# Kernel optimization log

Measured on AMD Instinct MI355X. Metric: run time of the kernel, lower is better.

## Reference

```python
import jax, jax.numpy as jnp
import numpy as np

HEADS, DH = 8, 64  # SelfAttention defaults: heads=8, dim_head=64


def _layernorm(x, g, b, eps=1e-5):
    mu = x.mean(-1, keepdims=True)
    var = ((x - mu) ** 2).mean(-1, keepdims=True)
    return (x - mu) / jnp.sqrt(var + eps) * g + b


def setup_inputs() -> dict:
    key = jax.random.key(0)
    ks = jax.random.split(key, 13)
    B, H, W, D, P = 1, 256, 256, 64, 128
    inner = HEADS * DH
    s = 0.05  # weight scale to keep logits in a sane range
    return {
        "x": jax.random.normal(ks[0], (B, H, W, D), jnp.float32),
        "pair_bias": jax.random.normal(ks[1], (B, W, W, P), jnp.float32),
        "Wq_w": jax.random.normal(ks[2], (D, inner), jnp.float32) * s,
        "Wkv_w": jax.random.normal(ks[3], (D, 2 * inner), jnp.float32) * s,
        "Wout_w": jax.random.normal(ks[4], (inner, D), jnp.float32) * s,
        "bout_w": jnp.zeros((D,), jnp.float32),
        "Wq_h": jax.random.normal(ks[5], (D, inner), jnp.float32) * s,
        "Wkv_h": jax.random.normal(ks[6], (D, 2 * inner), jnp.float32) * s,
        "Wout_h": jax.random.normal(ks[7], (inner, D), jnp.float32) * s,
        "bout_h": jnp.zeros((D,), jnp.float32),
        "pair_ln_g": jnp.ones((P,), jnp.float32),
        "pair_ln_b": jnp.zeros((P,), jnp.float32),
        "W_pair": jax.random.normal(ks[8], (P, HEADS), jnp.float32) * s,
    }


def _qkv(x2d, Wq, Wkv):
    # x2d: (N, L, D) -> q, k, v each (N, heads, L, dh)
    N, L, _ = x2d.shape
    q = (x2d @ Wq).reshape(N, L, HEADS, DH).transpose(0, 2, 1, 3)
    kv = (x2d @ Wkv).reshape(N, L, 2, HEADS, DH)
    k = kv[:, :, 0].transpose(0, 2, 1, 3)
    v = kv[:, :, 1].transpose(0, 2, 1, 3)
    return q, k, v


def reference(x, pair_bias, Wq_w, Wkv_w, Wout_w, bout_w,
              Wq_h, Wkv_h, Wout_h, bout_h, pair_ln_g, pair_ln_b, W_pair):
    B, H, W, D = x.shape  # B=1, H=n_seqs, W=length, D=dim
    scale = DH ** -0.5

    # ---- width attention: attend over seq dim H, batched per column (b*w) ----
    xw = jnp.transpose(x, (0, 2, 1, 3)).reshape(B * W, H, D)
    q, k, v = _qkv(xw, Wq_w, Wkv_w)
    dots = jnp.einsum('bhid,bhjd->bhij', q, k) * scale  # (B*W, heads, H, H)
    attn = jax.nn.softmax(dots, axis=-1)
    ow = jnp.einsum('bhij,bhjd->bhid', attn, v)
    ow = ow.transpose(0, 2, 1, 3).reshape(B * W, H, HEADS * DH)
    ow = ow @ Wout_w + bout_w
    w_out = ow.reshape(B, W, H, D).transpose(0, 2, 1, 3)  # (B, H, W, D)

    # ---- height attention: tied over seq dim (tie_attn_dim=H), pair bias ----
    xh = x.reshape(B * H, W, D)
    q, k, v = _qkv(xh, Wq_h, Wkv_h)           # (B*H, heads, W, dh)
    q = q.reshape(B, H, HEADS, W, DH)
    k = k.reshape(B, H, HEADS, W, DH)
    v = v.reshape(B, H, HEADS, W, DH)
    dots = jnp.einsum('brhid,brhjd->bhij', q, k) * scale * (H ** -0.5)  # (B, heads, W, W)
    pb = _layernorm(pair_bias, pair_ln_g, pair_ln_b) @ W_pair  # (B, W, W, heads)
    dots = dots + pb.transpose(0, 3, 1, 2)
    attn = jax.nn.softmax(dots, axis=-1)
    oh = jnp.einsum('bhij,brhjd->brhid', attn, v)  # (B, H, heads, W, dh)
    oh = oh.transpose(0, 1, 3, 2, 4).reshape(B, H, W, HEADS * DH)
    h_out = oh @ Wout_h + bout_h  # (B, H, W, D)

    return (w_out + h_out) * 0.5
```

## Files before the change

### kernel.cpp

```cpp
#include <hip/hip_runtime.h>
#include <hip/hip_bf16.h>

typedef __hip_bfloat16 bf16;
typedef __attribute__((ext_vector_type(8))) short bf16x8;
typedef __attribute__((ext_vector_type(4))) float f32x4;

#define MFMA16(a, b, c) __builtin_amdgcn_mfma_f32_16x16x32_bf16(a, b, c, 0, 0, 0)

#define HH 256
#define WW 256
#define NHEADS 8
#define NROWS 65536


__device__ __forceinline__ bf16x8 cvt8(const float* f) {
  bf16x8 r;
  bf16* h = (bf16*)&r;
#pragma unroll
  for (int i = 0; i < 8; i++) h[i] = __float2bfloat16(f[i]);
  return r;
}

__global__ void __launch_bounds__(256) k_wt1(const float* __restrict__ Wq,
                                             const float* __restrict__ Wkv,
                                             bf16* __restrict__ Wt) {
  const int idx = blockIdx.x * 256 + threadIdx.x;
  const int k = idx / 1536, c = idx - k * 1536;
  const float val = (c < 512) ? Wq[k * 512 + c] : Wkv[k * 1024 + (c - 512)];
  Wt[(size_t)c * 64 + k] = __float2bfloat16(val);
}

__global__ void __launch_bounds__(256) k_wo(const float* __restrict__ Wout_w,
                                            const float* __restrict__ Wout_h,
                                            bf16* __restrict__ Wo_w,
                                            bf16* __restrict__ Wo_h) {
  int idx = blockIdx.x * 256 + threadIdx.x;
  const float* W = Wout_w;
  bf16* dst = Wo_w;
  if (idx >= 32768) { idx -= 32768; W = Wout_h; dst = Wo_h; }
  const int c = idx >> 9, d = idx & 511;
  dst[idx] = __float2bfloat16(W[d * 64 + c]);
}

__global__ void __launch_bounds__(256) k_qkv_mfma(const float* __restrict__ x,
                                                  const bf16* __restrict__ Wt,
                                                  bf16* __restrict__ d0,
                                                  bf16* __restrict__ d1,
                                                  bf16* __restrict__ d2,
                                                  int swap, int cg_lo, int cg_hi) {
  __shared__ __align__(16) bf16 Cs[64 * 136];
  const int tid = threadIdx.x, lane = tid & 63, wv = tid >> 6;
  const int m16 = lane & 15, kq = lane >> 4;
  const int rowA = blockIdx.x * 64 + wv * 16 + m16;

  const float* xr = x + (size_t)rowA * 64;
  float xf[8];
  bf16x8 af[2];
  *(float4*)&xf[0] = *(const float4*)(xr + kq * 8);
  *(float4*)&xf[4] = *(const float4*)(xr + kq * 8 + 4);
  af[0] = cvt8(xf);
  *(float4*)&xf[0] = *(const float4*)(xr + 32 + kq * 8);
  *(float4*)&xf[4] = *(const float4*)(xr + 32 + kq * 8 + 4);
  af[1] = cvt8(xf);

  size_t wrow[4];
#pragma unroll
  for (int s = 0; s < 4; s++) {
    const int row = (s * 256 + tid) >> 4;
    const int rc = blockIdx.x * 64 + row;
    const int rr = swap ? (((rc & 255) << 8) | (rc >> 8)) : rc;
    wrow[s] = (size_t)rr * 512;
  }
  const int ccol = (tid & 15) * 8;
  const int lrow0 = wv * 16 + kq * 4;

#pragma unroll 1
  for (int cg = cg_lo; cg < cg_hi; cg++) {
    bf16* dst = (cg < 4) ? d0 : (cg < 8) ? d1 : d2;
    const int cbase = (cg & 3) * 128;
#pragma unroll
    for (int ct = 0; ct < 8; ct++) {
      const bf16* wp = Wt + (size_t)(cg * 128 + ct * 16 + m16) * 64 + kq * 8;
      const bf16x8 b0 = *(const bf16x8*)wp;
      const bf16x8 b1 = *(const bf16x8*)(wp + 32);
      f32x4 a = (f32x4){0.f, 0.f, 0.f, 0.f};
      a = MFMA16(af[0], b0, a);
      a = MFMA16(af[1], b1, a);
#pragma unroll
      for (int r = 0; r < 4; r++)
        Cs[(lrow0 + r) * 136 + ct * 16 + m16] = __float2bfloat16(a[r]);
    }
    __syncthreads();
#pragma unroll
    for (int s = 0; s < 4; s++) {
      const int row = (s * 256 + tid) >> 4;
      *(uint4*)(dst + wrow[s] + cbase + ccol) = *(const uint4*)&Cs[row * 136 + ccol];
    }
    __syncthreads();
  }
}

__global__ void __launch_bounds__(256, 2)
k_width_fused(const float* __restrict__ x, const bf16* __restrict__ Wt,
              bf16* __restrict__ Ow) {
  __shared__ __align__(16) char smem[65536];
  bf16* Qs = (bf16*)smem;
  bf16* Ks = (bf16*)(smem + 32768);
  bf16* Vt = (bf16*)(smem + 49152);
  const int w = blockIdx.x, head = blockIdx.y;
  const int tid = threadIdx.x, lane = tid & 63, wv = tid >> 6;
  bf16* Ps = (bf16*)(smem + wv * 5120);
  const int m16 = lane & 15, kq = lane >> 4;
  const int i0 = wv * 64;

  bf16x8 af[4][2];
#pragma unroll
  for (int mt = 0; mt < 4; mt++) {
    const float* xr = x + ((size_t)((i0 + mt * 16 + m16) * 256 + w)) * 64;
    float xf[8];
    *(float4*)&xf[0] = *(const float4*)(xr + kq * 8);
    *(float4*)&xf[4] = *(const float4*)(xr + kq * 8 + 4);
    af[mt][0] = cvt8(xf);
    *(float4*)&xf[0] = *(const float4*)(xr + 32 + kq * 8);
    *(float4*)&xf[4] = *(const float4*)(xr + 32 + kq * 8 + 4);
    af[mt][1] = cvt8(xf);
  }
#pragma unroll
  for (int nt = 0; nt < 4; nt++) {
    const bf16* wp = Wt + (size_t)(head * 64 + nt * 16 + m16) * 64 + kq * 8;
    const bf16x8 w0 = *(const bf16x8*)wp;
    const bf16x8 w1 = *(const bf16x8*)(wp + 32);
#pragma unroll
    for (int mt = 0; mt < 4; mt++) {
      f32x4 a = (f32x4){0.f, 0.f, 0.f, 0.f};
      a = MFMA16(af[mt][0], w0, a);
      a = MFMA16(af[mt][1], w1, a);
#pragma unroll
      for (int r = 0; r < 4; r++) {
        const int i = i0 + mt * 16 + kq * 4 + r;
        const int d = nt * 16 + m16;
        Qs[i * 64 + (((d >> 3) ^ (i & 7)) << 3) + (d & 7)] = __float2bfloat16(a[r]);
      }
    }
  }
  __syncthreads();
  bf16x8 qf[4][2];
#pragma unroll
  for (int it = 0; it < 4; it++)
#pragma unroll
    for (int ks = 0; ks < 2; ks++)
      qf[it][ks] = *(const bf16x8*)&Qs[(i0 + it * 16 + m16) * 64 +
                                       (((ks * 4 + kq) ^ (m16 & 7)) << 3)];

  f32x4 acc[4][4];
#pragma unroll
  for (int a = 0; a < 4; a++)
#pragma unroll
    for (int b = 0; b < 4; b++) acc[a][b] = (f32x4){0.f, 0.f, 0.f, 0.f};
  float rsum[4][4];
#pragma unroll
  for (int a = 0; a < 4; a++)
#pragma unroll
    for (int r = 0; r < 4; r++) rsum[a][r] = 0.f;

#pragma unroll 1
  for (int half = 0; half < 2; half++) {
    if (half) __syncthreads();
    bf16x8 afk[2][2];
#pragma unroll
    for (int mt = 0; mt < 2; mt++) {
      const int jrow = half * 128 + wv * 32 + mt * 16 + m16;
      const float* xr = x + ((size_t)(jrow * 256 + w)) * 64;
      float xf[8];
      *(float4*)&xf[0] = *(const float4*)(xr + kq * 8);
      *(float4*)&xf[4] = *(const float4*)(xr + kq * 8 + 4);
      afk[mt][0] = cvt8(xf);
      *(float4*)&xf[0] = *(const float4*)(xr + 32 + kq * 8);
      *(float4*)&xf[4] = *(const float4*)(xr + 32 + kq * 8 + 4);
      afk[mt][1] = cvt8(xf);
    }
#pragma unroll
    for (int nt = 0; nt < 4; nt++) {
      const int d = nt * 16 + m16;
      {
        const bf16* wp = Wt + (size_t)(512 + head * 64 + d) * 64 + kq * 8;
        const bf16x8 w0 = *(const bf16x8*)wp;
        const bf16x8 w1 = *(const bf16x8*)(wp + 32);
#pragma unroll
        for (int mt = 0; mt < 2; mt++) {
          f32x4 a = (f32x4){0.f, 0.f, 0.f, 0.f};
          a = MFMA16(afk[mt][0], w0, a);
          a = MFMA16(afk[mt][1], w1, a);
#pragma unroll
          for (int r = 0; r < 4; r++) {
            const int jl = wv * 32 + mt * 16 + kq * 4 + r;
            Ks[jl * 64 + (((d >> 3) ^ (jl & 7)) << 3) + (d & 7)] = __float2bfloat16(a[r]);
          }
        }
      }
      {
        const bf16* wp = Wt + (size_t)(1024 + head * 64 + d) * 64 + kq * 8;
        const bf16x8 w0 = *(const bf16x8*)wp;
        const bf16x8 w1 = *(const bf16x8*)(wp + 32);
#pragma unroll
        for (int mt = 0; mt < 2; mt++) {
          f32x4 a = (f32x4){0.f, 0.f, 0.f, 0.f};
          a = MFMA16(afk[mt][0], w0, a);
          a = MFMA16(afk[mt][1], w1, a);
          const int jb = wv * 32 + mt * 16 + kq * 4;
          bf16 tmp[4];
#pragma unroll
          for (int r = 0; r < 4; r++) tmp[r] = __float2bfloat16(a[r]);
          *(uint2*)&Vt[d * 128 + (((jb >> 3) ^ (d & 7)) << 3) + (jb & 7)] =
              *(const uint2*)tmp;
        }
      }
    }
    __syncthreads();
#pragma unroll 1
    for (int jcl = 0; jcl < 4; jcl++) {
      bf16x8 kf[2][2];
#pragma unroll
      for (int jt = 0; jt < 2; jt++) {
        const int j = jcl * 32 + jt * 16 + m16;
#pragma unroll
        for (int ks = 0; ks < 2; ks++)
          kf[jt][ks] = *(const bf16x8*)&Ks[j * 64 + (((ks * 4 + kq) ^ (j & 7)) << 3)];
      }
#pragma unroll
      for (int it = 0; it < 4; it++)
#pragma unroll
        for (int jt = 0; jt < 2; jt++) {
          f32x4 s = (f32x4){0.f, 0.f, 0.f, 0.f};
          s = MFMA16(qf[it][0], kf[jt][0], s);
          s = MFMA16(qf[it][1], kf[jt][1], s);
#pragma unroll
          for (int r = 0; r < 4; r++) {
            float p = __expf(s[r] * 0.125f);
            rsum[it][r] += p;
            Ps[(it * 16 + kq * 4 + r) * 40 + jt * 16 + m16] = __float2bfloat16(p);
          }
        }
      bf16x8 pf[4], vf[4];
#pragma unroll
      for (int it = 0; it < 4; it++)
        pf[it] = *(const bf16x8*)&Ps[(it * 16 + m16) * 40 + kq * 8];
#pragma unroll
      for (int dt = 0; dt < 4; dt++)
        vf[dt] = *(const bf16x8*)&Vt[(dt * 16 + m16) * 128 +
                                     (((jcl * 4 + kq) ^ (m16 & 7)) << 3)];
#pragma unroll
      for (int it = 0; it < 4; it++)
#pragma unroll
        for (int dt = 0; dt < 4; dt++) acc[it][dt] = MFMA16(pf[it], vf[dt], acc[it][dt]);
    }
  }

#pragma unroll
  for (int it = 0; it < 4; it++)
#pragma unroll
    for (int r = 0; r < 4; r++) {
      float s = rsum[it][r];
      s += __shfl_xor(s, 1); s += __shfl_xor(s, 2);
      s += __shfl_xor(s, 4); s += __shfl_xor(s, 8);
      rsum[it][r] = 1.f / s;
    }
#pragma unroll
  for (int it = 0; it < 4; it++)
#pragma unroll
    for (int dt = 0; dt < 4; dt++)
#pragma unroll
      for (int r = 0; r < 4; r++) {
        const int i = i0 + it * 16 + kq * 4 + r;
        Ow[((size_t)(w * 256 + i)) * 512 + head * 64 + dt * 16 + m16] =
            __float2bfloat16(acc[it][dt][r] * rsum[it][r]);
      }
}

__global__ void __launch_bounds__(256, 2)
k_dots_s(const bf16* __restrict__ q, const bf16* __restrict__ kk, float* __restrict__ dp) {
  __shared__ __align__(16) bf16 Qs[64 * 72];
  __shared__ __align__(16) bf16 Ks[64 * 72];
  const int tile = blockIdx.x, head = blockIdx.y, rc = blockIdx.z;
  const int i0 = (tile >> 2) * 64, j0 = (tile & 3) * 64;
  const int tid = threadIdx.x, lane = tid & 63, wv = tid >> 6;
  const int m16 = lane & 15, kq = lane >> 4;
  float* slice = dp + (size_t)rc * 524288 + (size_t)head * 65536;

  f32x4 acc[4];
#pragma unroll
  for (int b = 0; b < 4; b++) acc[b] = (f32x4){0.f, 0.f, 0.f, 0.f};

  const int row = tid >> 2, ch = (tid & 3) * 16;
#pragma unroll 1
  for (int rr = 0; rr < 32; rr++) {
    const int rrow = rc * 32 + rr;
    __syncthreads();
    {
      const bf16* qsrc = q + ((size_t)(rrow * 256 + i0 + row) * 512 + head * 64 + ch);
      const bf16* ksrc = kk + ((size_t)(rrow * 256 + j0 + row) * 512 + head * 64 + ch);
      *(uint4*)&Qs[row * 72 + ch] = *(const uint4*)qsrc;
      *(uint4*)&Qs[row * 72 + ch + 8] = *(const uint4*)(qsrc + 8);
      *(uint4*)&Ks[row * 72 + ch] = *(const uint4*)ksrc;
      *(uint4*)&Ks[row * 72 + ch + 8] = *(const uint4*)(ksrc + 8);
    }
    __syncthreads();
#pragma unroll
    for (int ks = 0; ks < 2; ks++) {
      bf16x8 af = *(const bf16x8*)&Qs[(wv * 16 + m16) * 72 + ks * 32 + kq * 8];
      bf16x8 bfr[4];
#pragma unroll
      for (int jt = 0; jt < 4; jt++)
        bfr[jt] = *(const bf16x8*)&Ks[(jt * 16 + m16) * 72 + ks * 32 + kq * 8];
#pragma unroll
      for (int jt = 0; jt < 4; jt++) acc[jt] = MFMA16(af, bfr[jt], acc[jt]);
    }
  }
  const float sc = 1.f / 128.f;
#pragma unroll
  for (int jt = 0; jt < 4; jt++)
#pragma unroll
    for (int r = 0; r < 4; r++)
      slice[(size_t)(i0 + wv * 16 + kq * 4 + r) * 256 + j0 + jt * 16 + m16] = acc[jt][r] * sc;
}

__global__ void __launch_bounds__(256) k_pb(const float* __restrict__ pb,
                                            const float* __restrict__ g,
                                            const float* __restrict__ bb,
                                            const float* __restrict__ Wp,
                                            float* __restrict__ dots) {
  __shared__ float sn[4][128];
  const int tid = threadIdx.x, lane = tid & 63, wv = tid >> 6;
  const size_t ij = (size_t)blockIdx.x * 4 + wv;
  const float2 xv = *(const float2*)(pb + ij * 128 + lane * 2);

  float s = xv.x + xv.y;
#pragma unroll
  for (int o = 1; o < 64; o <<= 1) s += __shfl_xor(s, o);
  const float mu = s * (1.f / 128.f);
  const float d0 = xv.x - mu, d1 = xv.y - mu;
  float s2 = d0 * d0 + d1 * d1;
#pragma unroll
  for (int o = 1; o < 64; o <<= 1) s2 += __shfl_xor(s2, o);
  const float inv = rsqrtf(s2 * (1.f / 128.f) + 1e-5f);

  sn[wv][lane * 2 + 0] = d0 * inv * g[lane * 2 + 0] + bb[lane * 2 + 0];
  sn[wv][lane * 2 + 1] = d1 * inv * g[lane * 2 + 1] + bb[lane * 2 + 1];

  const int h = lane & 7, gp = lane >> 3;
  float a = 0.f;
#pragma unroll
  for (int p0 = 0; p0 < 16; p0++) {
    const int p = gp * 16 + p0;
    a += sn[wv][p] * Wp[p * 8 + h];
  }
  a += __shfl_xor(a, 8);
  a += __shfl_xor(a, 16);
  a += __shfl_xor(a, 32);
  if (lane < 8) dots[(size_t)h * 65536 + ij] += a;
}

__global__ void __launch_bounds__(256) k_softmax8(const float* __restrict__ dp,
                                                  bf16* __restrict__ P) {
  __shared__ float red[4];
  const int i = blockIdx.x, head = blockIdx.y, t = threadIdx.x;
  const size_t base = (size_t)head * 65536 + i * 256 + t;
  float lg = 0.f;
#pragma unroll
  for (int s = 0; s < 8; s++) lg += dp[(size_t)s * 524288 + base];
  const float e = __expf(lg);
  float s = e;
#pragma unroll
  for (int o = 1; o < 64; o <<= 1) s += __shfl_xor(s, o);
  if ((t & 63) == 0) red[t >> 6] = s;
  __syncthreads();
  const float S = red[0] + red[1] + red[2] + red[3];
  P[base] = __float2bfloat16(e / S);
}

__global__ void __launch_bounds__(256, 2)
k_h_pv_o(const bf16* __restrict__ P, const bf16* __restrict__ v, bf16* __restrict__ Oh) {
  __shared__ __align__(16) bf16 Vt[64 * 256];
  const int r = blockIdx.x, head = blockIdx.y;
  const int tid = threadIdx.x, lane = tid & 63, wv = tid >> 6;
  const int m16 = lane & 15, kq = lane >> 4;

  {
    const bf16* src = v + ((size_t)(r * 256 + tid) * 512 + head * 64);
    uint4 rr[8];
#pragma unroll
    for (int c = 0; c < 8; c++) rr[c] = ((const uint4*)src)[c];
    const int jl = tid & 7, jh = tid >> 3;
#pragma unroll
    for (int c = 0; c < 8; c++) {
      const bf16* e = (const bf16*)&rr[c];
#pragma unroll
      for (int t = 0; t < 8; t++) {
        const int d = c * 8 + t;
        Vt[d * 256 + ((jh ^ (d & 7)) << 3) + jl] = e[t];
      }
    }
  }

  const bf16* Pb = P + (size_t)head * 65536;
  const int i0 = wv * 64;
  auto loadP = [&](int ks, bf16x8 pf[4]) {
#pragma unroll
    for (int it = 0; it < 4; it++)
      pf[it] = *(const bf16x8*)(Pb + (size_t)(i0 + it * 16 + m16) * 256 + ks * 32 + kq * 8);
  };
  bf16x8 pcur[4];
  loadP(0, pcur);
  __syncthreads();

  f32x4 acc[4][4];
#pragma unroll
  for (int a = 0; a < 4; a++)
#pragma unroll
    for (int b = 0; b < 4; b++) acc[a][b] = (f32x4){0.f, 0.f, 0.f, 0.f};

#pragma unroll 1
  for (int ks = 0; ks < 8; ks++) {
    bf16x8 pnext[4];
    if (ks < 7) loadP(ks + 1, pnext);
    bf16x8 vf[4];
#pragma unroll
    for (int dt = 0; dt < 4; dt++)
      vf[dt] = *(const bf16x8*)&Vt[(dt * 16 + m16) * 256 + (((ks * 4 + kq) ^ (m16 & 7)) << 3)];
#pragma unroll
    for (int it = 0; it < 4; it++)
#pragma unroll
      for (int dt = 0; dt < 4; dt++) acc[it][dt] = MFMA16(pcur[it], vf[dt], acc[it][dt]);
    if (ks < 7) {
#pragma unroll
      for (int it = 0; it < 4; it++) pcur[it] = pnext[it];
    }
  }
#pragma unroll
  for (int it = 0; it < 4; it++)
#pragma unroll
    for (int dt = 0; dt < 4; dt++)
#pragma unroll
      for (int r2 = 0; r2 < 4; r2++) {
        const int i = i0 + it * 16 + kq * 4 + r2;
        Oh[((size_t)(r * 256 + i)) * 512 + head * 64 + dt * 16 + m16] =
            __float2bfloat16(acc[it][dt][r2]);
      }
}

__global__ void __launch_bounds__(256) k_outproj(const bf16* __restrict__ Ow,
                                                 const bf16* __restrict__ Oh,
                                                 const bf16* __restrict__ Wow,
                                                 const bf16* __restrict__ Woh,
                                                 const float* __restrict__ bw,
                                                 const float* __restrict__ bh,
                                                 float* __restrict__ out) {
  const int tid = threadIdx.x, lane = tid & 63, wv = tid >> 6;
  const int m16 = lane & 15, kq = lane >> 4;
  const int nA = blockIdx.x * 64 + wv * 16 + m16;
  const int wA = ((nA & 255) << 8) | (nA >> 8);

  const bf16* aw = Ow + (size_t)wA * 512 + kq * 8;
  const bf16* ah = Oh + (size_t)nA * 512 + kq * 8;

  f32x4 acc[4];
#pragma unroll
  for (int ct = 0; ct < 4; ct++) acc[ct] = (f32x4){0.f, 0.f, 0.f, 0.f};

#pragma unroll 1
  for (int kc = 0; kc < 16; kc++) {
    const bf16x8 afw = *(const bf16x8*)(aw + kc * 32);
    const bf16x8 afh = *(const bf16x8*)(ah + kc * 32);
#pragma unroll
    for (int ct = 0; ct < 4; ct++) {
      const bf16x8 bfw = *(const bf16x8*)(Wow + (size_t)(ct * 16 + m16) * 512 + kc * 32 + kq * 8);
      const bf16x8 bfh = *(const bf16x8*)(Woh + (size_t)(ct * 16 + m16) * 512 + kc * 32 + kq * 8);
      acc[ct] = MFMA16(afw, bfw, acc[ct]);
      acc[ct] = MFMA16(afh, bfh, acc[ct]);
    }
  }
  const int n0 = blockIdx.x * 64 + wv * 16 + kq * 4;
#pragma unroll
  for (int ct = 0; ct < 4; ct++) {
    const int c = ct * 16 + m16;
    const float bias = 0.5f * (bw[c] + bh[c]);
#pragma unroll
    for (int r = 0; r < 4; r++)
      out[(size_t)(n0 + r) * 64 + c] = 0.5f * acc[ct][r] + bias;
  }
}

extern "C" void kernel_launch(void* const* d_in, const int* in_sizes, int n_in,
                              void* d_out, int out_size, void* d_ws, size_t ws_size,
                              hipStream_t stream) {
  const float* x      = (const float*)d_in[0];
  const float* pair   = (const float*)d_in[1];
  const float* Wq_w   = (const float*)d_in[2];
  const float* Wkv_w  = (const float*)d_in[3];
  const float* Wout_w = (const float*)d_in[4];
  const float* bout_w = (const float*)d_in[5];
  const float* Wq_h   = (const float*)d_in[6];
  const float* Wkv_h  = (const float*)d_in[7];
  const float* Wout_h = (const float*)d_in[8];
  const float* bout_h = (const float*)d_in[9];
  const float* ln_g   = (const float*)d_in[10];
  const float* ln_b   = (const float*)d_in[11];
  const float* W_pair = (const float*)d_in[12];
  float* out = (float*)d_out;

  char* ws = (char*)d_ws;
  bf16* R0 = (bf16*)ws;
  bf16* R1 = (bf16*)(ws + 67108864);
  bf16* R2 = (bf16*)(ws + 134217728);
  bf16* Wt = (bf16*)(ws + 201326592);
  bf16* P  = (bf16*)(ws + 201326592 + 393216);
  bf16* Wo_w = (bf16*)(ws + 201326592 + 1441792);
  bf16* Wo_h = Wo_w + 32768;
  float* dp = out;

  k_wt1<<<384, 256, 0, stream>>>(Wq_w, Wkv_w, Wt);
  k_wo<<<256, 256, 0, stream>>>(Wout_w, Wout_h, Wo_w, Wo_h);
  k_width_fused<<<dim3(WW, NHEADS), 256, 0, stream>>>(x, Wt, R0);

  k_wt1<<<384, 256, 0, stream>>>(Wq_h, Wkv_h, Wt);
  k_qkv_mfma<<<1024, 256, 0, stream>>>(x, Wt, R1, R2, R1, 0, 0, 8);
  k_dots_s<<<dim3(16, NHEADS, 8), 256, 0, stream>>>(R1, R2, dp);
  k_qkv_mfma<<<1024, 256, 0, stream>>>(x, Wt, R1, R2, R1, 0, 8, 12);
  k_pb<<<65536 / 4, 256, 0, stream>>>(pair, ln_g, ln_b, W_pair, dp);
  k_softmax8<<<dim3(256, NHEADS), 256, 0, stream>>>(dp, P);
  k_h_pv_o<<<dim3(HH, NHEADS), 256, 0, stream>>>(P, R1, R2);

  k_outproj<<<1024, 256, 0, stream>>>(R0, R2, Wo_w, Wo_h, bout_w, bout_h, out);
}
```

Measured before the change: 546.9 us.

## Pre-transpose x to bf16 column-major and shrink width-attention K/V staging

Adds a pre-pass that converts x to bf16 and transposes it so each width column's 256 rows are contiguous. The width-attention kernel then reads each column with coalesced bf16 loads instead of strided fp32 loads followed by conversion. K/V are now produced in four chunks of 64 rows rather than two of 128, which cuts shared memory to 48KB so three blocks can run per CU. The cost is an extra kernel pass over x, a scratch buffer aliased onto R1, and an added barrier per chunk.

```diff
diff --git a/kernel.cpp b/kernel.cpp
--- a/kernel.cpp
+++ b/kernel.cpp
@@ -42,6 +42,21 @@
   dst[idx] = __float2bfloat16(W[d * 64 + c]);
 }
 
+__global__ void __launch_bounds__(256) k_xT(const float* __restrict__ x,
+                                            bf16* __restrict__ xT) {
+  const int tid = threadIdx.x, lane = tid & 63, wv = tid >> 6;
+  const int h = blockIdx.x >> 4;
+  const int w = (blockIdx.x & 15) * 16 + wv * 4 + (lane >> 4);
+  const int d0 = (lane & 15) * 4;
+  const float4 v = *(const float4*)(x + ((size_t)(h * 256 + w)) * 64 + d0);
+  bf16 tmp[4];
+  tmp[0] = __float2bfloat16(v.x);
+  tmp[1] = __float2bfloat16(v.y);
+  tmp[2] = __float2bfloat16(v.z);
+  tmp[3] = __float2bfloat16(v.w);
+  *(uint2*)(xT + ((size_t)(w * 256 + h)) * 64 + d0) = *(const uint2*)tmp;
+}
+
 __global__ void __launch_bounds__(256) k_qkv_mfma(const float* __restrict__ x,
                                                   const bf16* __restrict__ Wt,
                                                   bf16* __restrict__ d0,
@@ -100,30 +115,26 @@
   }
 }
 
-__global__ void __launch_bounds__(256, 2)
-k_width_fused(const float* __restrict__ x, const bf16* __restrict__ Wt,
+__global__ void __launch_bounds__(256, 3)
+k_width_fused(const bf16* __restrict__ xT, const bf16* __restrict__ Wt,
               bf16* __restrict__ Ow) {
-  __shared__ __align__(16) char smem[65536];
+  __shared__ __align__(16) char smem[49152];
   bf16* Qs = (bf16*)smem;
   bf16* Ks = (bf16*)(smem + 32768);
-  bf16* Vt = (bf16*)(smem + 49152);
+  bf16* Vt = (bf16*)(smem + 40960);
   const int w = blockIdx.x, head = blockIdx.y;
   const int tid = threadIdx.x, lane = tid & 63, wv = tid >> 6;
   bf16* Ps = (bf16*)(smem + wv * 5120);
   const int m16 = lane & 15, kq = lane >> 4;
   const int i0 = wv * 64;
+  const bf16* xcol = xT + (size_t)w * 256 * 64;
 
   bf16x8 af[4][2];
 #pragma unroll
   for (int mt = 0; mt < 4; mt++) {
-    const float* xr = x + ((size_t)((i0 + mt * 16 + m16) * 256 + w)) * 64;
-    float xf[8];
-    *(float4*)&xf[0] = *(const float4*)(xr + kq * 8);
-    *(float4*)&xf[4] = *(const float4*)(xr + kq * 8 + 4);
-    af[mt][0] = cvt8(xf);
-    *(float4*)&xf[0] = *(const float4*)(xr + 32 + kq * 8);
-    *(float4*)&xf[4] = *(const float4*)(xr + 32 + kq * 8 + 4);
-    af[mt][1] = cvt8(xf);
+    const bf16* xr = xcol + (size_t)(i0 + mt * 16 + m16) * 64 + kq * 8;
+    af[mt][0] = *(const bf16x8*)xr;
+    af[mt][1] = *(const bf16x8*)(xr + 32);
   }
 #pragma unroll
   for (int nt = 0; nt < 4; nt++) {
@@ -164,61 +175,47 @@
     for (int r = 0; r < 4; r++) rsum[a][r] = 0.f;
 
 #pragma unroll 1
-  for (int half = 0; half < 2; half++) {
-    if (half) __syncthreads();
-    bf16x8 afk[2][2];
-#pragma unroll
-    for (int mt = 0; mt < 2; mt++) {
-      const int jrow = half * 128 + wv * 32 + mt * 16 + m16;
-      const float* xr = x + ((size_t)(jrow * 256 + w)) * 64;
-      float xf[8];
-      *(float4*)&xf[0] = *(const float4*)(xr + kq * 8);
-      *(float4*)&xf[4] = *(const float4*)(xr + kq * 8 + 4);
-      afk[mt][0] = cvt8(xf);
-      *(float4*)&xf[0] = *(const float4*)(xr + 32 + kq * 8);
-      *(float4*)&xf[4] = *(const float4*)(xr + 32 + kq * 8 + 4);
-      afk[mt][1] = cvt8(xf);
-    }
-#pragma unroll
-    for (int nt = 0; nt < 4; nt++) {
-      const int d = nt * 16 + m16;
-      {
-        const bf16* wp = Wt + (size_t)(512 + head * 64 + d) * 64 + kq * 8;
-        const bf16x8 w0 = *(const bf16x8*)wp;
-        const bf16x8 w1 = *(const bf16x8*)(wp + 32);
-#pragma unroll
-        for (int mt = 0; mt < 2; mt++) {
+  for (int g = 0; g < 4; g++) {
+    {
+      const int jrow = g * 64 + wv * 16 + m16;
+      const bf16* xr = xcol + (size_t)jrow * 64 + kq * 8;
+      const bf16x8 ak0 = *(const bf16x8*)xr;
+      const bf16x8 ak1 = *(const bf16x8*)(xr + 32);
+#pragma unroll
+      for (int nt = 0; nt < 4; nt++) {
+        const int d = nt * 16 + m16;
+        {
+          const bf16* wp = Wt + (size_t)(512 + head * 64 + d) * 64 + kq * 8;
+          const bf16x8 w0 = *(const bf16x8*)wp;
+          const bf16x8 w1 = *(const bf16x8*)(wp + 32);
           f32x4 a = (f32x4){0.f, 0.f, 0.f, 0.f};
-          a = MFMA16(afk[mt][0], w0, a);
-          a = MFMA16(afk[mt][1], w1, a);
+          a = MFMA16(ak0, w0, a);
+          a = MFMA16(ak1, w1, a);
 #pragma unroll
           for (int r = 0; r < 4; r++) {
-            const int jl = wv * 32 + mt * 16 + kq * 4 + r;
+            const int jl = wv * 16 + kq * 4 + r;
             Ks[jl * 64 + (((d >> 3) ^ (jl & 7)) << 3) + (d & 7)] = __float2bfloat16(a[r]);
           }
         }
-      }
-      {
-        const bf16* wp = Wt + (size_t)(1024 + head * 64 + d) * 64 + kq * 8;
-        const bf16x8 w0 = *(const bf16x8*)wp;
-        const bf16x8 w1 = *(const bf16x8*)(wp + 32);
-#pragma unroll
-        for (int mt = 0; mt < 2; mt++) {
+        {
+          const bf16* wp = Wt + (size_t)(1024 + head * 64 + d) * 64 + kq * 8;
+          const bf16x8 w0 = *(const bf16x8*)wp;
+          const bf16x8 w1 = *(const bf16x8*)(wp + 32);
           f32x4 a = (f32x4){0.f, 0.f, 0.f, 0.f};
-          a = MFMA16(afk[mt][0], w0, a);
-          a = MFMA16(afk[mt][1], w1, a);
-          const int jb = wv * 32 + mt * 16 + kq * 4;
+          a = MFMA16(ak0, w0, a);
+          a = MFMA16(ak1, w1, a);
+          const int jb = wv * 16 + kq * 4;
           bf16 tmp[4];
 #pragma unroll
           for (int r = 0; r < 4; r++) tmp[r] = __float2bfloat16(a[r]);
-          *(uint2*)&Vt[d * 128 + (((jb >> 3) ^ (d & 7)) << 3) + (jb & 7)] =
+          *(uint2*)&Vt[d * 64 + (((jb >> 3) ^ (d & 7)) << 3) + (jb & 7)] =
               *(const uint2*)tmp;
         }
       }
     }
     __syncthreads();
-#pragma unroll 1
-    for (int jcl = 0; jcl < 4; jcl++) {
+#pragma unroll
+    for (int jcl = 0; jcl < 2; jcl++) {
       bf16x8 kf[2][2];
 #pragma unroll
       for (int jt = 0; jt < 2; jt++) {
@@ -247,13 +244,14 @@
         pf[it] = *(const bf16x8*)&Ps[(it * 16 + m16) * 40 + kq * 8];
 #pragma unroll
       for (int dt = 0; dt < 4; dt++)
-        vf[dt] = *(const bf16x8*)&Vt[(dt * 16 + m16) * 128 +
+        vf[dt] = *(const bf16x8*)&Vt[(dt * 16 + m16) * 64 +
                                      (((jcl * 4 + kq) ^ (m16 & 7)) << 3)];
 #pragma unroll
       for (int it = 0; it < 4; it++)
 #pragma unroll
         for (int dt = 0; dt < 4; dt++) acc[it][dt] = MFMA16(pf[it], vf[dt], acc[it][dt]);
     }
+    __syncthreads();
   }
 
 #pragma unroll
@@ -516,11 +514,13 @@
   bf16* P  = (bf16*)(ws + 201326592 + 393216);
   bf16* Wo_w = (bf16*)(ws + 201326592 + 1441792);
   bf16* Wo_h = Wo_w + 32768;
+  bf16* xT = R1;
   float* dp = out;
 
   k_wt1<<<384, 256, 0, stream>>>(Wq_w, Wkv_w, Wt);
   k_wo<<<256, 256, 0, stream>>>(Wout_w, Wout_h, Wo_w, Wo_h);
-  k_width_fused<<<dim3(WW, NHEADS), 256, 0, stream>>>(x, Wt, R0);
+  k_xT<<<4096, 256, 0, stream>>>(x, xT);
+  k_width_fused<<<dim3(WW, NHEADS), 256, 0, stream>>>(xT, Wt, R0);
 
   k_wt1<<<384, 256, 0, stream>>>(Wq_h, Wkv_h, Wt);
   k_qkv_mfma<<<1024, 256, 0, stream>>>(x, Wt, R1, R2, R1, 0, 0, 8);
```

Result: slower. 703.7 us (+28.7%).

## Fuse height-attention QKV projection into dots and PV kernels

Applied to the files above, without the earlier changes.

Removes the standalone QKV projection kernel for height attention and computes Q/K projections on the fly inside the dots kernel and V projection inside the PV kernel, reading x and bf16 weights directly. This avoids writing and rereading large bf16 Q/K/V intermediates in global memory. In exchange Q and K rows are recomputed redundantly across tiles and the dots loop gains MFMA and conversion work per iteration.

```diff
diff --git a/kernel.cpp b/kernel.cpp
--- a/kernel.cpp
+++ b/kernel.cpp
@@ -40,64 +40,6 @@
   if (idx >= 32768) { idx -= 32768; W = Wout_h; dst = Wo_h; }
   const int c = idx >> 9, d = idx & 511;
   dst[idx] = __float2bfloat16(W[d * 64 + c]);
-}
-
-__global__ void __launch_bounds__(256) k_qkv_mfma(const float* __restrict__ x,
-                                                  const bf16* __restrict__ Wt,
-                                                  bf16* __restrict__ d0,
-                                                  bf16* __restrict__ d1,
-                                                  bf16* __restrict__ d2,
-                                                  int swap, int cg_lo, int cg_hi) {
-  __shared__ __align__(16) bf16 Cs[64 * 136];
-  const int tid = threadIdx.x, lane = tid & 63, wv = tid >> 6;
-  const int m16 = lane & 15, kq = lane >> 4;
-  const int rowA = blockIdx.x * 64 + wv * 16 + m16;
-
-  const float* xr = x + (size_t)rowA * 64;
-  float xf[8];
-  bf16x8 af[2];
-  *(float4*)&xf[0] = *(const float4*)(xr + kq * 8);
-  *(float4*)&xf[4] = *(const float4*)(xr + kq * 8 + 4);
-  af[0] = cvt8(xf);
-  *(float4*)&xf[0] = *(const float4*)(xr + 32 + kq * 8);
-  *(float4*)&xf[4] = *(const float4*)(xr + 32 + kq * 8 + 4);
-  af[1] = cvt8(xf);
-
-  size_t wrow[4];
-#pragma unroll
-  for (int s = 0; s < 4; s++) {
-    const int row = (s * 256 + tid) >> 4;
-    const int rc = blockIdx.x * 64 + row;
-    const int rr = swap ? (((rc & 255) << 8) | (rc >> 8)) : rc;
-    wrow[s] = (size_t)rr * 512;
-  }
-  const int ccol = (tid & 15) * 8;
-  const int lrow0 = wv * 16 + kq * 4;
-
-#pragma unroll 1
-  for (int cg = cg_lo; cg < cg_hi; cg++) {
-    bf16* dst = (cg < 4) ? d0 : (cg < 8) ? d1 : d2;
-    const int cbase = (cg & 3) * 128;
-#pragma unroll
-    for (int ct = 0; ct < 8; ct++) {
-      const bf16* wp = Wt + (size_t)(cg * 128 + ct * 16 + m16) * 64 + kq * 8;
-      const bf16x8 b0 = *(const bf16x8*)wp;
-      const bf16x8 b1 = *(const bf16x8*)(wp + 32);
-      f32x4 a = (f32x4){0.f, 0.f, 0.f, 0.f};
-      a = MFMA16(af[0], b0, a);
-      a = MFMA16(af[1], b1, a);
-#pragma unroll
-      for (int r = 0; r < 4; r++)
-        Cs[(lrow0 + r) * 136 + ct * 16 + m16] = __float2bfloat16(a[r]);
-    }
-    __syncthreads();
-#pragma unroll
-    for (int s = 0; s < 4; s++) {
-      const int row = (s * 256 + tid) >> 4;
-      *(uint4*)(dst + wrow[s] + cbase + ccol) = *(const uint4*)&Cs[row * 136 + ccol];
-    }
-    __syncthreads();
-  }
 }
 
 __global__ void __launch_bounds__(256, 2)
@@ -278,7 +220,7 @@
 }
 
 __global__ void __launch_bounds__(256, 2)
-k_dots_s(const bf16* __restrict__ q, const bf16* __restrict__ kk, float* __restrict__ dp) {
+k_dots_f(const float* __restrict__ x, const bf16* __restrict__ Wt, float* __restrict__ dp) {
   __shared__ __align__(16) bf16 Qs[64 * 72];
   __shared__ __align__(16) bf16 Ks[64 * 72];
   const int tile = blockIdx.x, head = blockIdx.y, rc = blockIdx.z;
@@ -287,22 +229,52 @@
   const int m16 = lane & 15, kq = lane >> 4;
   float* slice = dp + (size_t)rc * 524288 + (size_t)head * 65536;
 
+  const bf16* WtQ = Wt + (size_t)(head * 64) * 64 + kq * 8;
+  const bf16* WtK = Wt + (size_t)(512 + head * 64) * 64 + kq * 8;
+
   f32x4 acc[4];
 #pragma unroll
   for (int b = 0; b < 4; b++) acc[b] = (f32x4){0.f, 0.f, 0.f, 0.f};
 
-  const int row = tid >> 2, ch = (tid & 3) * 16;
+  const int lrow = wv * 16 + kq * 4;
+
 #pragma unroll 1
   for (int rr = 0; rr < 32; rr++) {
-    const int rrow = rc * 32 + rr;
+    const int rbase = (rc * 32 + rr) * 256;
     __syncthreads();
     {
-      const bf16* qsrc = q + ((size_t)(rrow * 256 + i0 + row) * 512 + head * 64 + ch);
-      const bf16* ksrc = kk + ((size_t)(rrow * 256 + j0 + row) * 512 + head * 64 + ch);
-      *(uint4*)&Qs[row * 72 + ch] = *(const uint4*)qsrc;
-      *(uint4*)&Qs[row * 72 + ch + 8] = *(const uint4*)(qsrc + 8);
-      *(uint4*)&Ks[row * 72 + ch] = *(const uint4*)ksrc;
-      *(uint4*)&Ks[row * 72 + ch + 8] = *(const uint4*)(ksrc + 8);
+      const float* xr = x + (size_t)(rbase + i0 + wv * 16 + m16) * 64;
+      float xf[8];
+      bf16x8 qa0, qa1, ka0, ka1;
+      *(float4*)&xf[0] = *(const float4*)(xr + kq * 8);
+      *(float4*)&xf[4] = *(const float4*)(xr + kq * 8 + 4);
+      qa0 = cvt8(xf);
+      *(float4*)&xf[0] = *(const float4*)(xr + 32 + kq * 8);
+      *(float4*)&xf[4] = *(const float4*)(xr + 32 + kq * 8 + 4);
+      qa1 = cvt8(xf);
+      const float* yr = x + (size_t)(rbase + j0 + wv * 16 + m16) * 64;
+      *(float4*)&xf[0] = *(const float4*)(yr + kq * 8);
+      *(float4*)&xf[4] = *(const float4*)(yr + kq * 8 + 4);
+      ka0 = cvt8(xf);
+      *(float4*)&xf[0] = *(const float4*)(yr + 32 + kq * 8);
+      *(float4*)&xf[4] = *(const float4*)(yr + 32 + kq * 8 + 4);
+      ka1 = cvt8(xf);
+#pragma unroll
+      for (int nt = 0; nt < 4; nt++) {
+        const bf16* wq = WtQ + (size_t)(nt * 16 + m16) * 64;
+        f32x4 aq = (f32x4){0.f, 0.f, 0.f, 0.f};
+        aq = MFMA16(qa0, *(const bf16x8*)wq, aq);
+        aq = MFMA16(qa1, *(const bf16x8*)(wq + 32), aq);
+        const bf16* wk = WtK + (size_t)(nt * 16 + m16) * 64;
+        f32x4 ak = (f32x4){0.f, 0.f, 0.f, 0.f};
+        ak = MFMA16(ka0, *(const bf16x8*)wk, ak);
+        ak = MFMA16(ka1, *(const bf16x8*)(wk + 32), ak);
+#pragma unroll
+        for (int r = 0; r < 4; r++) {
+          Qs[(lrow + r) * 72 + nt * 16 + m16] = __float2bfloat16(aq[r]);
+          Ks[(lrow + r) * 72 + nt * 16 + m16] = __float2bfloat16(ak[r]);
+        }
+      }
     }
     __syncthreads();
 #pragma unroll
@@ -379,25 +351,39 @@
 }
 
 __global__ void __launch_bounds__(256, 2)
-k_h_pv_o(const bf16* __restrict__ P, const bf16* __restrict__ v, bf16* __restrict__ Oh) {
+k_h_pv_f(const bf16* __restrict__ P, const float* __restrict__ x,
+         const bf16* __restrict__ Wt, bf16* __restrict__ Oh) {
   __shared__ __align__(16) bf16 Vt[64 * 256];
   const int r = blockIdx.x, head = blockIdx.y;
   const int tid = threadIdx.x, lane = tid & 63, wv = tid >> 6;
   const int m16 = lane & 15, kq = lane >> 4;
 
   {
-    const bf16* src = v + ((size_t)(r * 256 + tid) * 512 + head * 64);
-    uint4 rr[8];
-#pragma unroll
-    for (int c = 0; c < 8; c++) rr[c] = ((const uint4*)src)[c];
-    const int jl = tid & 7, jh = tid >> 3;
-#pragma unroll
-    for (int c = 0; c < 8; c++) {
-      const bf16* e = (const bf16*)&rr[c];
-#pragma unroll
-      for (int t = 0; t < 8; t++) {
-        const int d = c * 8 + t;
-        Vt[d * 256 + ((jh ^ (d & 7)) << 3) + jl] = e[t];
+    const bf16* WtV = Wt + (size_t)(1024 + head * 64) * 64 + kq * 8;
+#pragma unroll
+    for (int mt = 0; mt < 4; mt++) {
+      const int jb16 = wv * 64 + mt * 16;
+      const float* xr = x + (size_t)(r * 256 + jb16 + m16) * 64;
+      float xf[8];
+      bf16x8 a0, a1;
+      *(float4*)&xf[0] = *(const float4*)(xr + kq * 8);
+      *(float4*)&xf[4] = *(const float4*)(xr + kq * 8 + 4);
+      a0 = cvt8(xf);
+      *(float4*)&xf[0] = *(const float4*)(xr + 32 + kq * 8);
+      *(float4*)&xf[4] = *(const float4*)(xr + 32 + kq * 8 + 4);
+      a1 = cvt8(xf);
+#pragma unroll
+      for (int nt = 0; nt < 4; nt++) {
+        const int d = nt * 16 + m16;
+        const bf16* wp = WtV + (size_t)(nt * 16 + m16) * 64;
+        f32x4 a = (f32x4){0.f, 0.f, 0.f, 0.f};
+        a = MFMA16(a0, *(const bf16x8*)wp, a);
+        a = MFMA16(a1, *(const bf16x8*)(wp + 32), a);
+        const int j = jb16 + kq * 4;
+        bf16 tmp[4];
+#pragma unroll
+        for (int r2 = 0; r2 < 4; r2++) tmp[r2] = __float2bfloat16(a[r2]);
+        *(uint2*)&Vt[d * 256 + (((j >> 3) ^ (d & 7)) << 3) + (j & 7)] = *(const uint2*)tmp;
       }
     }
   }
@@ -510,7 +496,6 @@
 
   char* ws = (char*)d_ws;
   bf16* R0 = (bf16*)ws;
-  bf16* R1 = (bf16*)(ws + 67108864);
   bf16* R2 = (bf16*)(ws + 134217728);
   bf16* Wt = (bf16*)(ws + 201326592);
   bf16* P  = (bf16*)(ws + 201326592 + 393216);
@@ -523,12 +508,10 @@
   k_width_fused<<<dim3(WW, NHEADS), 256, 0, stream>>>(x, Wt, R0);
 
   k_wt1<<<384, 256, 0, stream>>>(Wq_h, Wkv_h, Wt);
-  k_qkv_mfma<<<1024, 256, 0, stream>>>(x, Wt, R1, R2, R1, 0, 0, 8);
-  k_dots_s<<<dim3(16, NHEADS, 8), 256, 0, stream>>>(R1, R2, dp);
-  k_qkv_mfma<<<1024, 256, 0, stream>>>(x, Wt, R1, R2, R1, 0, 8, 12);
+  k_dots_f<<<dim3(16, NHEADS, 8), 256, 0, stream>>>(x, Wt, dp);
   k_pb<<<65536 / 4, 256, 0, stream>>>(pair, ln_g, ln_b, W_pair, dp);
   k_softmax8<<<dim3(256, NHEADS), 256, 0, stream>>>(dp, P);
-  k_h_pv_o<<<dim3(HH, NHEADS), 256, 0, stream>>>(P, R1, R2);
+  k_h_pv_f<<<dim3(HH, NHEADS), 256, 0, stream>>>(P, x, Wt, R2);
 
   k_outproj<<<1024, 256, 0, stream>>>(R0, R2, Wo_w, Wo_h, bout_w, bout_h, out);
 }
```

New measurement: 526.4 us. 1.04x faster.
